# Performance work log

Hardware: AMD Instinct MI355X
Metric: run time of the kernel (lower is better)

Reference implementation:

```python
import jax, jax.numpy as jnp
import numpy as np

B, N, IN, HID, OUT = 64, 256, 7, 64, 32
DEG = 32
NT = B * N          # total nodes per side
E = NT * DEG        # intra-graph edges per side
TAU = 1.0
MAX_ITER = 10
EPS = 1e-5          # InstanceNorm2d eps


def setup_inputs() -> dict:
    key = jax.random.key(0)
    ks = jax.random.split(key, 12)

    def edges(k):
        # random intra-graph edges: local indices in [0, N) plus per-graph offset
        loc = jax.random.randint(k, (2, B, N * DEG), 0, N)
        off = (jnp.arange(B) * N)[None, :, None]
        return (loc + off).reshape(2, -1).astype(jnp.int64)

    def lin(k, fi, fo):
        return jax.random.normal(k, (fi, fo), jnp.float32) / np.float32(np.sqrt(fi))

    return {
        "x1": jax.random.normal(ks[0], (NT, IN), jnp.float32),
        "x2": jax.random.normal(ks[1], (NT, IN), jnp.float32),
        "edge1": edges(ks[2]),
        "edge2": edges(ks[3]),
        "Wl1": lin(ks[4], IN, HID), "Wr1": lin(ks[5], IN, HID),
        "bl1": jnp.zeros((HID,), jnp.float32), "br1": jnp.zeros((HID,), jnp.float32),
        "att1": jax.random.normal(ks[6], (HID,), jnp.float32) * 0.1,
        "bias1": jnp.zeros((HID,), jnp.float32),
        "Wl2": lin(ks[7], HID, OUT), "Wr2": lin(ks[8], HID, OUT),
        "bl2": jnp.zeros((OUT,), jnp.float32), "br2": jnp.zeros((OUT,), jnp.float32),
        "att2": jax.random.normal(ks[9], (OUT,), jnp.float32) * 0.1,
        "bias2": jnp.zeros((OUT,), jnp.float32),
        "gamma": jnp.ones((1,), jnp.float32),
        "beta": jnp.zeros((1,), jnp.float32),
    }


def _gatv2(x, src, dst, Wl, bl, Wr, br, att, bias):
    # PyG GATv2Conv, heads=1: score = att . leaky_relu(lin_l(x_j) + lin_r(x_i))
    xl = x @ Wl + bl  # source transform
    xr = x @ Wr + br  # target transform
    e = jax.nn.leaky_relu(xl[src] + xr[dst], 0.2)     # [E, D]
    score = e @ att                                    # [E]
    smax = jax.ops.segment_max(score, dst, num_segments=NT)
    ex = jnp.exp(score - smax[dst])
    den = jax.ops.segment_sum(ex, dst, num_segments=NT)
    alpha = ex / den[dst]
    out = jax.ops.segment_sum(alpha[:, None] * xl[src], dst, num_segments=NT)
    return out + bias


def _encode(x, edge, params):
    # add self loops (PyG add_self_loops=True default)
    loops = jnp.arange(NT)
    src = jnp.concatenate([edge[0], loops])
    dst = jnp.concatenate([edge[1], loops])
    h = jax.nn.relu(_gatv2(x, src, dst, *params[0]))
    return _gatv2(h, src, dst, *params[1])


def _soft_topk(sim_n):
    # AFAT-style differentiable top-k: OT between flattened scores and
    # {min, max} anchors with marginals [(n-k)/n, k/n], k = N2 per pair.
    n = N * N
    k = N
    flat = sim_n.reshape(B, n)
    mn = flat.min(axis=1, keepdims=True)
    mx = flat.max(axis=1, keepdims=True)
    dist = jnp.stack([flat - mn, mx - flat], axis=-1)  # [B, n, 2] (|s-min|,|s-max|)
    logK = -dist / TAU
    log_row = -jnp.log(jnp.float32(n))
    log_col = jnp.log(jnp.array([(n - k) / n, k / n], jnp.float32))
    for i in range(MAX_ITER):
        if i % 2 == 0:  # row normalization to uniform 1/n
            logK = logK - jax.scipy.special.logsumexp(logK, axis=-1, keepdims=True) + log_row
        else:           # column normalization to [(n-k)/n, k/n]
            logK = logK - jax.scipy.special.logsumexp(logK, axis=1, keepdims=True) + log_col[None, None, :]
    soft = jnp.clip(jnp.exp(logK[:, :, 1]) * n, 0.0, 1.0)  # selection probability per entry
    return soft.reshape(B, N, N)


def reference(x1, x2, edge1, edge2, Wl1, Wr1, bl1, br1, att1, bias1,
              Wl2, Wr2, bl2, br2, att2, bias2, gamma, beta):
    params = ((Wl1, bl1, Wr1, br1, att1, bias1), (Wl2, bl2, Wr2, br2, att2, bias2))
    h1 = _encode(x1, edge1, params).reshape(B, N, OUT)
    h2 = _encode(x2, edge2, params).reshape(B, N, OUT)
    sim = jnp.einsum('bnd,bmd->bnm', h1, h2)
    # InstanceNorm2d(1, affine=True): normalize each pair's sim matrix
    mu = sim.mean(axis=(1, 2), keepdims=True)
    var = sim.var(axis=(1, 2), keepdims=True)
    sim_n = gamma[0] * (sim - mu) * jax.lax.rsqrt(var + EPS) + beta[0]
    return _soft_topk(sim_n)  # soft_S stacked over the batch, [B, N, N]
```

## Files before the change

### kernel.cpp

```cpp
#include <hip/hip_runtime.h>

#define NB 64
#define NN 256
#define IND 7
#define HIDD 64
#define OUTD 32
#define EPG 8192
#define ETOT 524288
#define CAPQ 2600
#define SRCPAD 2624

typedef _Float16 f16;
typedef f16 f16x2 __attribute__((ext_vector_type(2)));
typedef f16 f16x4 __attribute__((ext_vector_type(4)));
typedef f16 f16x8 __attribute__((ext_vector_type(8)));
typedef float f32x4 __attribute__((ext_vector_type(4)));

__device__ __forceinline__ float bsum16(float v, float* rb){
#pragma unroll
  for (int o = 32; o > 0; o >>= 1) v += __shfl_xor(v, o, 64);
  __syncthreads();
  if ((threadIdx.x & 63) == 0) rb[threadIdx.x >> 6] = v;
  __syncthreads();
  float s = 0.f;
#pragma unroll
  for (int i = 0; i < 16; i++) s += rb[i];
  return s;
}
__device__ __forceinline__ float bmin16(float v, float* rb){
#pragma unroll
  for (int o = 32; o > 0; o >>= 1) v = fminf(v, __shfl_xor(v, o, 64));
  __syncthreads();
  if ((threadIdx.x & 63) == 0) rb[threadIdx.x >> 6] = v;
  __syncthreads();
  float s = rb[0];
#pragma unroll
  for (int i = 1; i < 16; i++) s = fminf(s, rb[i]);
  return s;
}
__device__ __forceinline__ float bmax16(float v, float* rb){
#pragma unroll
  for (int o = 32; o > 0; o >>= 1) v = fmaxf(v, __shfl_xor(v, o, 64));
  __syncthreads();
  if ((threadIdx.x & 63) == 0) rb[threadIdx.x >> 6] = v;
  __syncthreads();
  float s = rb[0];
#pragma unroll
  for (int i = 1; i < 16; i++) s = fmaxf(s, rb[i]);
  return s;
}

__device__ __forceinline__ f16x2 lrelu2(f16x2 s){
  const f16x2 k = {(f16)0.2f, (f16)0.2f};
  return __builtin_elementwise_max(s, s * k);
}
__device__ __forceinline__ f16x2 shfl_h2(f16x2 v, int lane){
  int i = __builtin_bit_cast(int, v);
  i = __shfl(i, lane, 64);
  return __builtin_bit_cast(f16x2, i);
}

__global__ __launch_bounds__(512, 4) void gat1(
    const float* __restrict__ x1, const float* __restrict__ x2,
    const int* __restrict__ e1, const int* __restrict__ e2,
    const float* __restrict__ Wl, const float* __restrict__ Wr,
    const float* __restrict__ bl, const float* __restrict__ br,
    const float* __restrict__ att, const float* __restrict__ bias,
    f16* __restrict__ hmid,
    int* __restrict__ meta, unsigned char* __restrict__ srcs)
{
  __shared__ __align__(16) f16 xl_s[256 * 72];
  __shared__ float sc_s[CAPQ];
  __shared__ unsigned int src_su[SRCPAD / 4];
  __shared__ int deg_s[64], start_s[64], cnt_s[64];
  unsigned char* src_s = (unsigned char*)src_su;

  const int bid = blockIdx.x;
  const int gs = bid >> 2, lo = (bid & 3) * 64;
  const int side = gs >> 6, g = gs & 63;
  const float* x = side ? x2 : x1;
  const int* eb = side ? e2 : e1;
  const int* es = eb + g * EPG;
  const int* ed = eb + ETOT + g * EPG;
  const int t = threadIdx.x;

  if (t < 64) deg_s[t] = 0;

  {
    const int node = t >> 1, dh = t & 1;
    float xv[IND];
    const float* xr_ = x + (g * 256 + node) * IND;
#pragma unroll
    for (int k = 0; k < IND; k++) xv[k] = xr_[k];
#pragma unroll
    for (int ch = 0; ch < 4; ch++){
      f16x8 o;
#pragma unroll
      for (int j = 0; j < 8; j++){
        int dd = dh * 32 + ch * 8 + j;
        float a = bl[dd];
#pragma unroll
        for (int k = 0; k < IND; k++) a = fmaf(xv[k], Wl[k * HIDD + dd], a);
        o[j] = (f16)a;
      }
      *(f16x8*)&xl_s[node * 72 + dh * 32 + ch * 8] = o;
    }
  }

  const int pairi = t >> 3, sub = t & 7, ln = lo + pairi;
  f16x2 m[4], am[4];
  {
    float xv[IND];
    const float* xq = x + (g * 256 + ln) * IND;
#pragma unroll
    for (int k = 0; k < IND; k++) xv[k] = xq[k];
#pragma unroll
    for (int c = 0; c < 4; c++){
#pragma unroll
      for (int u = 0; u < 2; u++){
        int dd = sub * 8 + 2 * c + u;
        float a = br[dd];
#pragma unroll
        for (int k = 0; k < IND; k++) a = fmaf(xv[k], Wr[k * HIDD + dd], a);
        m[c][u] = (f16)a;
        am[c][u] = (f16)att[dd];
      }
    }
  }
  f16x2 xrh[32], atth[32];
  {
    const int base = (t & 63) & ~7;
#pragma unroll
    for (int ss = 0; ss < 8; ss++){
#pragma unroll
      for (int c = 0; c < 4; c++){
        xrh[ss * 4 + c] = shfl_h2(m[c], base + ss);
        atth[ss * 4 + c] = shfl_h2(am[c], base + ss);
      }
    }
  }
  __syncthreads();

  for (int e = t; e < EPG + 256; e += 512){
    int dl = (e < EPG) ? (ed[e] & 255) : (e - EPG);
    int r = dl - lo;
    if ((unsigned)r < 64u) atomicAdd(&deg_s[r], 1);
  }
  __syncthreads();
  if (t < 64){
    int v = deg_s[t], s = v;
#pragma unroll
    for (int off = 1; off < 64; off <<= 1){
      int u = __shfl_up(s, off, 64);
      if (t >= off) s += u;
    }
    start_s[t] = s - v;
    cnt_s[t] = s - v;
    meta[bid * 128 + t] = s - v;
    meta[bid * 128 + 64 + t] = v;
  }
  __syncthreads();
  for (int e = t; e < EPG + 256; e += 512){
    int sl, dl;
    if (e < EPG){ sl = es[e] & 255; dl = ed[e] & 255; }
    else { sl = dl = e - EPG; }
    int r = dl - lo;
    if ((unsigned)r < 64u){
      int p = atomicAdd(&cnt_s[r], 1);
      if (p < CAPQ) src_s[p] = (unsigned char)sl;
    }
  }
  __syncthreads();
  {
    int ttl = start_s[63] + deg_s[63];
    if (ttl > CAPQ) ttl = CAPQ;
    unsigned int* gsrc = (unsigned int*)(srcs + (size_t)bid * SRCPAD);
    int nw = (ttl + 3) >> 2;
    for (int i = t; i < nw; i += 512) gsrc[i] = src_su[i];
  }

  const int s0 = start_s[pairi];
  int sE = s0 + deg_s[pairi];
  if (sE > CAPQ) sE = CAPQ;
  float lmax = -3.0e38f;
  for (int idx = s0 + sub; idx < sE; idx += 8){
    int sl = src_s[idx];
    const f16x8* rp = (const f16x8*)&xl_s[(unsigned)sl * 72];
    float accs[4] = {0.f, 0.f, 0.f, 0.f};
#pragma unroll
    for (int blk = 0; blk < 8; blk++){
      f16x8 rv = rp[blk];
#pragma unroll
      for (int u = 0; u < 4; u++){
        f16x2 v = {rv[2 * u], rv[2 * u + 1]};
        v = v + xrh[blk * 4 + u];
        accs[u] = __builtin_amdgcn_fdot2(lrelu2(v), atth[blk * 4 + u], accs[u], false);
      }
    }
    float sc = (accs[0] + accs[1]) + (accs[2] + accs[3]);
    sc_s[idx] = sc;
    lmax = fmaxf(lmax, sc);
  }
  lmax = fmaxf(lmax, __shfl_xor(lmax, 1, 64));
  lmax = fmaxf(lmax, __shfl_xor(lmax, 2, 64));
  lmax = fmaxf(lmax, __shfl_xor(lmax, 4, 64));
  const float smax = lmax;
  float ssum = 0.f;
  for (int idx = s0 + sub; idx < sE; idx += 8){
    float w = __expf(sc_s[idx] - smax);
    ssum += w;
    sc_s[idx] = w;
  }
  ssum += __shfl_xor(ssum, 1, 64);
  ssum += __shfl_xor(ssum, 2, 64);
  ssum += __shfl_xor(ssum, 4, 64);
  float inv = 1.f / ssum;
  float acc[8];
#pragma unroll
  for (int c = 0; c < 8; c++) acc[c] = 0.f;
  {
    int sl = (s0 < sE) ? src_s[s0] : 0;
    f16x8 row = *(const f16x8*)&xl_s[(unsigned)sl * 72 + sub * 8];
    for (int idx = s0; idx < sE; idx++){
      int sln = (idx + 1 < sE) ? src_s[idx + 1] : 0;
      f16x8 rown = *(const f16x8*)&xl_s[(unsigned)sln * 72 + sub * 8];
      float w = sc_s[idx];
#pragma unroll
      for (int c = 0; c < 8; c++) acc[c] = fmaf(w, (float)row[c], acc[c]);
      row = rown;
    }
  }
  f16x8 o;
#pragma unroll
  for (int c = 0; c < 8; c++)
    o[c] = (f16)fmaxf(acc[c] * inv + bias[sub * 8 + c], 0.f);
  *(f16x8*)(hmid + (size_t)(gs * 256 + ln) * 64 + sub * 8) = o;
}

__global__ __launch_bounds__(512, 4) void gat2(
    const int* __restrict__ meta, const unsigned char* __restrict__ srcs,
    const f16* __restrict__ hmid,
    const float* __restrict__ Wl, const float* __restrict__ Wr,
    const float* __restrict__ bl, const float* __restrict__ br,
    const float* __restrict__ att, const float* __restrict__ bias,
    f16* __restrict__ hout)
{
  __shared__ __align__(16) f16 xl_s[256 * 40];
  __shared__ __align__(16) f16 xr_s[64 * 40];
  __shared__ float sc_s[CAPQ];
  __shared__ unsigned int src_su[SRCPAD / 4];
  __shared__ int start_s[64], deg_s[64];
  unsigned char* src_s = (unsigned char*)src_su;

  const int bid = blockIdx.x;
  const int gs = bid >> 2, lo = (bid & 3) * 64;
  const int t = threadIdx.x;

  if (t < 64){
    start_s[t] = meta[bid * 128 + t];
    deg_s[t] = meta[bid * 128 + 64 + t];
  }
  {
    int ttl = meta[bid * 128 + 63] + meta[bid * 128 + 64 + 63];
    if (ttl > CAPQ) ttl = CAPQ;
    const unsigned int* gsrc = (const unsigned int*)(srcs + (size_t)bid * SRCPAD);
    int nw = (ttl + 3) >> 2;
    for (int i = t; i < nw; i += 512) src_su[i] = gsrc[i];
  }

  {
    const int w = t >> 6, lane = t & 63;
    const int m = lane & 15, quad = lane >> 4;
    f16x8 a[2][2];
#pragma unroll
    for (int ti = 0; ti < 2; ti++){
      const f16* arow = hmid + (size_t)(gs * 256 + (2 * w + ti) * 16 + m) * 64;
      a[ti][0] = *(const f16x8*)(arow + quad * 8);
      a[ti][1] = *(const f16x8*)(arow + 32 + quad * 8);
    }
#pragma unroll
    for (int H = 0; H < 2; H++){
      const int n = H * 16 + m;
      f16x8 b0, b1;
#pragma unroll
      for (int j = 0; j < 8; j++){
        b0[j] = (f16)Wl[(quad * 8 + j) * 32 + n];
        b1[j] = (f16)Wl[(32 + quad * 8 + j) * 32 + n];
      }
      const float bv = bl[n];
#pragma unroll
      for (int ti = 0; ti < 2; ti++){
        f32x4 acc = {0.f, 0.f, 0.f, 0.f};
        acc = __builtin_amdgcn_mfma_f32_16x16x32_f16(a[ti][0], b0, acc, 0, 0, 0);
        acc = __builtin_amdgcn_mfma_f32_16x16x32_f16(a[ti][1], b1, acc, 0, 0, 0);
#pragma unroll
        for (int r = 0; r < 4; r++)
          xl_s[((2 * w + ti) * 16 + quad * 4 + r) * 40 + n] = (f16)(acc[r] + bv);
      }
    }
    if (w < 4){
      const f16* arow = hmid + (size_t)(gs * 256 + lo + w * 16 + m) * 64;
      f16x8 c0 = *(const f16x8*)(arow + quad * 8);
      f16x8 c1 = *(const f16x8*)(arow + 32 + quad * 8);
#pragma unroll
      for (int H = 0; H < 2; H++){
        const int n = H * 16 + m;
        f16x8 b0, b1;
#pragma unroll
        for (int j = 0; j < 8; j++){
          b0[j] = (f16)Wr[(quad * 8 + j) * 32 + n];
          b1[j] = (f16)Wr[(32 + quad * 8 + j) * 32 + n];
        }
        const float bv = br[n];
        f32x4 acc = {0.f, 0.f, 0.f, 0.f};
        acc = __builtin_amdgcn_mfma_f32_16x16x32_f16(c0, b0, acc, 0, 0, 0);
        acc = __builtin_amdgcn_mfma_f32_16x16x32_f16(c1, b1, acc, 0, 0, 0);
#pragma unroll
        for (int r = 0; r < 4; r++)
          xr_s[(w * 16 + quad * 4 + r) * 40 + n] = (f16)(acc[r] + bv);
      }
    }
  }
  __syncthreads();

  const int pairi = t >> 3, sub = t & 7, ln = lo + pairi;
  f16x2 xrh[16], atth[16];
  {
    const f16x8* xrp = (const f16x8*)&xr_s[pairi * 40];
#pragma unroll
    for (int q = 0; q < 4; q++){
      f16x8 v = xrp[q];
#pragma unroll
      for (int u = 0; u < 4; u++){
        xrh[q * 4 + u][0] = v[2 * u];
        xrh[q * 4 + u][1] = v[2 * u + 1];
      }
    }
#pragma unroll
    for (int i = 0; i < 16; i++){
      atth[i][0] = (f16)att[2 * i];
      atth[i][1] = (f16)att[2 * i + 1];
    }
  }

  const int s0 = start_s[pairi];
  int sE = s0 + deg_s[pairi];
  if (sE > CAPQ) sE = CAPQ;
  float lmax = -3.0e38f;
  for (int idx = s0 + sub; idx < sE; idx += 8){
    int sl = src_s[idx];
    const f16x8* rp = (const f16x8*)&xl_s[(unsigned)sl * 40];
    float accs[4] = {0.f, 0.f, 0.f, 0.f};
#pragma unroll
    for (int blk = 0; blk < 4; blk++){
      f16x8 rv = rp[blk];
#pragma unroll
      for (int u = 0; u < 4; u++){
        f16x2 v = {rv[2 * u], rv[2 * u + 1]};
        v = v + xrh[blk * 4 + u];
        accs[u] = __builtin_amdgcn_fdot2(lrelu2(v), atth[blk * 4 + u], accs[u], false);
      }
    }
    float sc = (accs[0] + accs[1]) + (accs[2] + accs[3]);
    sc_s[idx] = sc;
    lmax = fmaxf(lmax, sc);
  }
  lmax = fmaxf(lmax, __shfl_xor(lmax, 1, 64));
  lmax = fmaxf(lmax, __shfl_xor(lmax, 2, 64));
  lmax = fmaxf(lmax, __shfl_xor(lmax, 4, 64));
  const float smax = lmax;
  float ssum = 0.f;
  for (int idx = s0 + sub; idx < sE; idx += 8){
    float w = __expf(sc_s[idx] - smax);
    ssum += w;
    sc_s[idx] = w;
  }
  ssum += __shfl_xor(ssum, 1, 64);
  ssum += __shfl_xor(ssum, 2, 64);
  ssum += __shfl_xor(ssum, 4, 64);
  float inv = 1.f / ssum;

  float acc[4];
#pragma unroll
  for (int c = 0; c < 4; c++) acc[c] = 0.f;
  {
    int sl = (s0 < sE) ? src_s[s0] : 0;
    f16x4 row = *(const f16x4*)&xl_s[(unsigned)sl * 40 + sub * 4];
    for (int idx = s0; idx < sE; idx++){
      int sln = (idx + 1 < sE) ? src_s[idx + 1] : 0;
      f16x4 rown = *(const f16x4*)&xl_s[(unsigned)sln * 40 + sub * 4];
      float w = sc_s[idx];
#pragma unroll
      for (int c = 0; c < 4; c++) acc[c] = fmaf(w, (float)row[c], acc[c]);
      row = rown;
    }
  }
  f16x4 o;
#pragma unroll
  for (int c = 0; c < 4; c++)
    o[c] = (f16)(acc[c] * inv + bias[sub * 4 + c]);
  *(f16x4*)(hout + (size_t)(gs * 256 + ln) * 32 + sub * 4) = o;
}

__global__ __launch_bounds__(1024) void simtopk(
    const f16* __restrict__ H,
    const float* __restrict__ gamma, const float* __restrict__ beta,
    float* __restrict__ out)
{
  __shared__ float rb[16];
  __shared__ unsigned int hist[8192];
  const int b = blockIdx.x, t = threadIdx.x;
  const int w = t >> 6, lane = t & 63;
  const int m = lane & 15, quad = lane >> 4;

  const f16* h1 = H + (size_t)b * 256 * 32;
  const f16* h2 = H + (size_t)(64 + b) * 256 * 32;

  f16x8 av = *(const f16x8*)(h1 + (size_t)(w * 16 + m) * 32 + quad * 8);
  f32x4 c[16];
#pragma unroll
  for (int j = 0; j < 16; j++){
    f16x8 bv = *(const f16x8*)(h2 + (size_t)(j * 16 + m) * 32 + quad * 8);
    f32x4 z = {0.f, 0.f, 0.f, 0.f};
    c[j] = __builtin_amdgcn_mfma_f32_16x16x32_f16(av, bv, z, 0, 0, 0);
  }

  float sm = 0.f, s2 = 0.f, mn = 3.0e38f, mx = -3.0e38f;
#pragma unroll
  for (int j = 0; j < 16; j++)
#pragma unroll
    for (int r = 0; r < 4; r++){
      float s = c[j][r];
      sm += s; s2 = fmaf(s, s, s2);
      mn = fminf(mn, s); mx = fmaxf(mx, s);
    }
  sm = bsum16(sm, rb);
  s2 = bsum16(s2, rb);
  mn = bmin16(mn, rb);
  mx = bmax16(mx, rb);

  const float mu = sm * (1.f / 65536.f);
  const float var = s2 * (1.f / 65536.f) - mu * mu;
  const float a = gamma[0] * rsqrtf(var + 1e-5f);
  const float cc = beta[0] - a * mu;
  float mnn = a * mn + cc, mxn = a * mx + cc;
  if (a < 0.f){ float tmp = mnn; mnn = mxn; mxn = tmp; }
  const float al = 2.f * a;
  const float be = 2.f * cc - mnn - mxn;
  const float R = fmaxf(mxn - mnn, 1e-12f);
  const float binscale = 4096.f / R;

  for (int i = t; i < 8192; i += 1024) hist[i] = 0u;
  __syncthreads();
#pragma unroll
  for (int j = 0; j < 16; j++)
#pragma unroll
    for (int r = 0; r < 4; r++){
      float z = fmaf(al, c[j][r], be);
      int bi = (int)fmaf(z, binscale, 4096.f);
      bi = min(max(bi, 0), 8191);
      atomicAdd(&hist[bi], 1u);
      c[j][r] = __expf(-z);
    }
  __syncthreads();

  const float wbin = R * (1.f / 4096.f);
  float ebs[8];
#pragma unroll
  for (int j = 0; j < 8; j++){
    float zc = fmaf((float)(t * 8 + j) + 0.5f, wbin, -R);
    ebs[j] = __expf(-zc);
  }
  float cnts[8];
#pragma unroll
  for (int j = 0; j < 8; j++) cnts[j] = (float)hist[t * 8 + j];

  float D = 0.f, S = 256.f, eD = 1.f;
  for (int p = 0; p < 5; p++){
    float loc = 0.f;
#pragma unroll
    for (int j = 0; j < 8; j++)
      loc += cnts[j] / (1.f + ebs[j] * eD);
    S = bsum16(loc, rb);
    if (p < 4){
      D += -5.5412635f  + __logf(65536.f - S) - __logf(S);
      eD = __expf(-D);
    }
  }

  const float scale = 256.f / S;
  float* ob = out + (size_t)b * 65536;
#pragma unroll
  for (int j = 0; j < 16; j++){
#pragma unroll
    for (int r = 0; r < 4; r++){
      float v = scale / (1.f + c[j][r] * eD);
      int row = w * 16 + quad * 4 + r;
      int col = j * 16 + m;
      ob[row * 256 + col] = fminf(v, 1.f);
    }
  }
}

extern "C" void kernel_launch(void* const* d_in, const int* in_sizes, int n_in,
                              void* d_out, int out_size, void* d_ws, size_t ws_size,
                              hipStream_t stream)
{
  const float* x1   = (const float*)d_in[0];
  const float* x2   = (const float*)d_in[1];
  const int*   e1   = (const int*)d_in[2];
  const int*   e2   = (const int*)d_in[3];
  const float* Wl1  = (const float*)d_in[4];
  const float* Wr1  = (const float*)d_in[5];
  const float* bl1  = (const float*)d_in[6];
  const float* br1  = (const float*)d_in[7];
  const float* att1 = (const float*)d_in[8];
  const float* bias1= (const float*)d_in[9];
  const float* Wl2  = (const float*)d_in[10];
  const float* Wr2  = (const float*)d_in[11];
  const float* bl2  = (const float*)d_in[12];
  const float* br2  = (const float*)d_in[13];
  const float* att2 = (const float*)d_in[14];
  const float* bias2= (const float*)d_in[15];
  const float* gamma= (const float*)d_in[16];
  const float* beta = (const float*)d_in[17];

  char* ws = (char*)d_ws;
  f16* hmid = (f16*)ws;
  f16* hfin = (f16*)(ws + (size_t)4 * 1024 * 1024);
  int* meta = (int*)(ws + (size_t)6 * 1024 * 1024);
  unsigned char* srcs = (unsigned char*)(ws + (size_t)6 * 1024 * 1024 + 512 * 128 * 4);
  float* out = (float*)d_out;

  gat1<<<512, 512, 0, stream>>>(x1, x2, e1, e2, Wl1, Wr1, bl1, br1, att1, bias1,
                                hmid, meta, srcs);
  gat2<<<512, 512, 0, stream>>>(meta, srcs, hmid, Wl2, Wr2, bl2, br2, att2, bias2, hfin);
  simtopk<<<64, 1024, 0, stream>>>(hfin, gamma, beta, out);
}
```

Measured before the change: 188.1 us.

## Split sim/topk into multi-kernel pipeline and degree-sort destination nodes in GAT

The single 64-block sim+Sinkhorn kernel becomes three stages: a 256-block matmul kernel that writes raw similarities and atomically combines per-batch statistics, a histogram/Sinkhorn-solve kernel that reads sim back, and a 512-block elementwise output kernel. The aim is to use more CUs than 64 blocks could. In exchange the 16 MB output is written, read and rewritten through global memory, with extra launches and a zeroing kernel. The GAT kernels also cache edge indices in registers so edges are read from global memory once. They sort destination nodes by degree so that the 8-lane groups sharing a wavefront have similar work, reducing divergence.

```diff
diff --git a/kernel.cpp b/kernel.cpp
--- a/kernel.cpp
+++ b/kernel.cpp
@@ -58,6 +58,14 @@
   int i = __builtin_bit_cast(int, v);
   i = __shfl(i, lane, 64);
   return __builtin_bit_cast(f16x2, i);
+}
+__device__ __forceinline__ unsigned fkey(float f){
+  unsigned b = __float_as_uint(f);
+  return (b & 0x80000000u) ? ~b : (b | 0x80000000u);
+}
+__device__ __forceinline__ float fkinv(unsigned k){
+  unsigned b = (k & 0x80000000u) ? (k ^ 0x80000000u) : ~k;
+  return __uint_as_float(b);
 }
 
 __global__ __launch_bounds__(512, 4) void gat1(
@@ -73,6 +81,7 @@
   __shared__ float sc_s[CAPQ];
   __shared__ unsigned int src_su[SRCPAD / 4];
   __shared__ int deg_s[64], start_s[64], cnt_s[64];
+  __shared__ unsigned char perm[64];
   unsigned char* src_s = (unsigned char*)src_su;
 
   const int bid = blockIdx.x;
@@ -86,6 +95,20 @@
 
   if (t < 64) deg_s[t] = 0;
 
+  unsigned short epk[17];
+  int nE = 0;
+#pragma unroll
+  for (int i = 0; i < 17; i++){
+    int e = t + i * 512;
+    if (e < EPG + 256){
+      int sl, dl;
+      if (e < EPG){ sl = es[e] & 255; dl = ed[e] & 255; }
+      else { sl = dl = e - EPG; }
+      epk[i] = (unsigned short)((dl << 8) | sl);
+      nE = i + 1;
+    }
+  }
+
   {
     const int node = t >> 1, dh = t & 1;
     float xv[IND];
@@ -106,44 +129,11 @@
       *(f16x8*)&xl_s[node * 72 + dh * 32 + ch * 8] = o;
     }
   }
-
-  const int pairi = t >> 3, sub = t & 7, ln = lo + pairi;
-  f16x2 m[4], am[4];
-  {
-    float xv[IND];
-    const float* xq = x + (g * 256 + ln) * IND;
-#pragma unroll
-    for (int k = 0; k < IND; k++) xv[k] = xq[k];
-#pragma unroll
-    for (int c = 0; c < 4; c++){
-#pragma unroll
-      for (int u = 0; u < 2; u++){
-        int dd = sub * 8 + 2 * c + u;
-        float a = br[dd];
-#pragma unroll
-        for (int k = 0; k < IND; k++) a = fmaf(xv[k], Wr[k * HIDD + dd], a);
-        m[c][u] = (f16)a;
-        am[c][u] = (f16)att[dd];
-      }
-    }
-  }
-  f16x2 xrh[32], atth[32];
-  {
-    const int base = (t & 63) & ~7;
-#pragma unroll
-    for (int ss = 0; ss < 8; ss++){
-#pragma unroll
-      for (int c = 0; c < 4; c++){
-        xrh[ss * 4 + c] = shfl_h2(m[c], base + ss);
-        atth[ss * 4 + c] = shfl_h2(am[c], base + ss);
-      }
-    }
-  }
-  __syncthreads();
-
-  for (int e = t; e < EPG + 256; e += 512){
-    int dl = (e < EPG) ? (ed[e] & 255) : (e - EPG);
-    int r = dl - lo;
+  __syncthreads();
+
+#pragma unroll
+  for (int i = 0; i < 17; i++) if (i < nE){
+    int r = (epk[i] >> 8) - lo;
     if ((unsigned)r < 64u) atomicAdd(&deg_s[r], 1);
   }
   __syncthreads();
@@ -158,16 +148,21 @@
     cnt_s[t] = s - v;
     meta[bid * 128 + t] = s - v;
     meta[bid * 128 + 64 + t] = v;
-  }
-  __syncthreads();
-  for (int e = t; e < EPG + 256; e += 512){
-    int sl, dl;
-    if (e < EPG){ sl = es[e] & 255; dl = ed[e] & 255; }
-    else { sl = dl = e - EPG; }
-    int r = dl - lo;
+    int r = 0;
+#pragma unroll 8
+    for (int j = 0; j < 64; j++){
+      int dj = deg_s[j];
+      r += (dj < v) || (dj == v && j < t);
+    }
+    perm[r] = (unsigned char)t;
+  }
+  __syncthreads();
+#pragma unroll
+  for (int i = 0; i < 17; i++) if (i < nE){
+    int dl = epk[i] >> 8, r = dl - lo;
     if ((unsigned)r < 64u){
       int p = atomicAdd(&cnt_s[r], 1);
-      if (p < CAPQ) src_s[p] = (unsigned char)sl;
+      if (p < CAPQ) src_s[p] = (unsigned char)(epk[i] & 255);
     }
   }
   __syncthreads();
@@ -177,6 +172,39 @@
     unsigned int* gsrc = (unsigned int*)(srcs + (size_t)bid * SRCPAD);
     int nw = (ttl + 3) >> 2;
     for (int i = t; i < nw; i += 512) gsrc[i] = src_su[i];
+  }
+
+  const int pairi = perm[t >> 3], sub = t & 7, ln = lo + pairi;
+  f16x2 m[4], am[4];
+  {
+    float xv[IND];
+    const float* xq = x + (g * 256 + ln) * IND;
+#pragma unroll
+    for (int k = 0; k < IND; k++) xv[k] = xq[k];
+#pragma unroll
+    for (int c = 0; c < 4; c++){
+#pragma unroll
+      for (int u = 0; u < 2; u++){
+        int dd = sub * 8 + 2 * c + u;
+        float a = br[dd];
+#pragma unroll
+        for (int k = 0; k < IND; k++) a = fmaf(xv[k], Wr[k * HIDD + dd], a);
+        m[c][u] = (f16)a;
+        am[c][u] = (f16)att[dd];
+      }
+    }
+  }
+  f16x2 xrh[32], atth[32];
+  {
+    const int base = (t & 63) & ~7;
+#pragma unroll
+    for (int ss = 0; ss < 8; ss++){
+#pragma unroll
+      for (int c = 0; c < 4; c++){
+        xrh[ss * 4 + c] = shfl_h2(m[c], base + ss);
+        atth[ss * 4 + c] = shfl_h2(am[c], base + ss);
+      }
+    }
   }
 
   const int s0 = start_s[pairi];
@@ -250,6 +278,7 @@
   __shared__ float sc_s[CAPQ];
   __shared__ unsigned int src_su[SRCPAD / 4];
   __shared__ int start_s[64], deg_s[64];
+  __shared__ unsigned char perm[64];
   unsigned char* src_s = (unsigned char*)src_su;
 
   const int bid = blockIdx.x;
@@ -322,8 +351,18 @@
     }
   }
   __syncthreads();
-
-  const int pairi = t >> 3, sub = t & 7, ln = lo + pairi;
+  if (t < 64){
+    int v = deg_s[t], r = 0;
+#pragma unroll 8
+    for (int j = 0; j < 64; j++){
+      int dj = deg_s[j];
+      r += (dj < v) || (dj == v && j < t);
+    }
+    perm[r] = (unsigned char)t;
+  }
+  __syncthreads();
+
+  const int pairi = perm[t >> 3], sub = t & 7, ln = lo + pairi;
   f16x2 xrh[16], atth[16];
   {
     const f16x8* xrp = (const f16x8*)&xr_s[pairi * 40];
@@ -402,45 +441,73 @@
   *(f16x4*)(hout + (size_t)(gs * 256 + ln) * 32 + sub * 4) = o;
 }
 
-__global__ __launch_bounds__(1024) void simtopk(
-    const f16* __restrict__ H,
+__global__ __launch_bounds__(256) void zerok(unsigned* __restrict__ stats){
+  int i = threadIdx.x;
+  if (i < 256) stats[i] = ((i & 3) == 2) ? 0xFFFFFFFFu : 0u;
+}
+
+__global__ __launch_bounds__(1024) void simk(
+    const f16* __restrict__ H, float* __restrict__ out,
+    unsigned* __restrict__ stats)
+{
+  __shared__ float rb[16];
+  const int b = blockIdx.x >> 2, q = blockIdx.x & 3, t = threadIdx.x;
+  const int w = t >> 6, lane = t & 63;
+  const int m = lane & 15, quad = lane >> 4;
+  const int rowT = q * 64 + (w & 3) * 16;
+  const int colB = (w >> 2) * 64;
+
+  const f16* h1 = H + (size_t)b * 256 * 32;
+  const f16* h2 = H + (size_t)(64 + b) * 256 * 32;
+
+  f16x8 av = *(const f16x8*)(h1 + (size_t)(rowT + m) * 32 + quad * 8);
+  f32x4 c[4];
+#pragma unroll
+  for (int jj = 0; jj < 4; jj++){
+    f16x8 bv = *(const f16x8*)(h2 + (size_t)(colB + jj * 16 + m) * 32 + quad * 8);
+    f32x4 z = {0.f, 0.f, 0.f, 0.f};
+    c[jj] = __builtin_amdgcn_mfma_f32_16x16x32_f16(av, bv, z, 0, 0, 0);
+  }
+
+  float sm = 0.f, s2 = 0.f, mn = 3.0e38f, mx = -3.0e38f;
+  float* ob = out + (size_t)b * 65536;
+#pragma unroll
+  for (int jj = 0; jj < 4; jj++)
+#pragma unroll
+    for (int r = 0; r < 4; r++){
+      float s = c[jj][r];
+      sm += s; s2 = fmaf(s, s, s2);
+      mn = fminf(mn, s); mx = fmaxf(mx, s);
+      ob[(rowT + quad * 4 + r) * 256 + colB + jj * 16 + m] = s;
+    }
+  sm = bsum16(sm, rb);
+  s2 = bsum16(s2, rb);
+  mn = bmin16(mn, rb);
+  mx = bmax16(mx, rb);
+  if (t == 0){
+    atomicAdd((float*)&stats[b * 4 + 0], sm);
+    atomicAdd((float*)&stats[b * 4 + 1], s2);
+    atomicMin(&stats[b * 4 + 2], fkey(mn));
+    atomicMax(&stats[b * 4 + 3], fkey(mx));
+  }
+}
+
+__global__ __launch_bounds__(1024) void sinkk(
+    const float* __restrict__ sim, const unsigned* __restrict__ stats,
     const float* __restrict__ gamma, const float* __restrict__ beta,
-    float* __restrict__ out)
+    float* __restrict__ res)
 {
   __shared__ float rb[16];
   __shared__ unsigned int hist[8192];
   const int b = blockIdx.x, t = threadIdx.x;
-  const int w = t >> 6, lane = t & 63;
-  const int m = lane & 15, quad = lane >> 4;
-
-  const f16* h1 = H + (size_t)b * 256 * 32;
-  const f16* h2 = H + (size_t)(64 + b) * 256 * 32;
-
-  f16x8 av = *(const f16x8*)(h1 + (size_t)(w * 16 + m) * 32 + quad * 8);
-  f32x4 c[16];
-#pragma unroll
-  for (int j = 0; j < 16; j++){
-    f16x8 bv = *(const f16x8*)(h2 + (size_t)(j * 16 + m) * 32 + quad * 8);
-    f32x4 z = {0.f, 0.f, 0.f, 0.f};
-    c[j] = __builtin_amdgcn_mfma_f32_16x16x32_f16(av, bv, z, 0, 0, 0);
-  }
-
-  float sm = 0.f, s2 = 0.f, mn = 3.0e38f, mx = -3.0e38f;
-#pragma unroll
-  for (int j = 0; j < 16; j++)
-#pragma unroll
-    for (int r = 0; r < 4; r++){
-      float s = c[j][r];
-      sm += s; s2 = fmaf(s, s, s2);
-      mn = fminf(mn, s); mx = fmaxf(mx, s);
-    }
-  sm = bsum16(sm, rb);
-  s2 = bsum16(s2, rb);
-  mn = bmin16(mn, rb);
-  mx = bmax16(mx, rb);
-
-  const float mu = sm * (1.f / 65536.f);
-  const float var = s2 * (1.f / 65536.f) - mu * mu;
+
+  const float sum = __uint_as_float(stats[b * 4 + 0]);
+  const float ssq = __uint_as_float(stats[b * 4 + 1]);
+  const float mn = fkinv(stats[b * 4 + 2]);
+  const float mx = fkinv(stats[b * 4 + 3]);
+
+  const float mu = sum * (1.f / 65536.f);
+  const float var = ssq * (1.f / 65536.f) - mu * mu;
   const float a = gamma[0] * rsqrtf(var + 1e-5f);
   const float cc = beta[0] - a * mu;
   float mnn = a * mn + cc, mxn = a * mx + cc;
@@ -452,28 +519,28 @@
 
   for (int i = t; i < 8192; i += 1024) hist[i] = 0u;
   __syncthreads();
-#pragma unroll
-  for (int j = 0; j < 16; j++)
-#pragma unroll
-    for (int r = 0; r < 4; r++){
-      float z = fmaf(al, c[j][r], be);
+  const f32x4* sp = (const f32x4*)(sim + (size_t)b * 65536);
+#pragma unroll
+  for (int k = 0; k < 16; k++){
+    f32x4 v = sp[k * 1024 + t];
+#pragma unroll
+    for (int u = 0; u < 4; u++){
+      float z = fmaf(al, v[u], be);
       int bi = (int)fmaf(z, binscale, 4096.f);
       bi = min(max(bi, 0), 8191);
       atomicAdd(&hist[bi], 1u);
-      c[j][r] = __expf(-z);
-    }
+    }
+  }
   __syncthreads();
 
   const float wbin = R * (1.f / 4096.f);
-  float ebs[8];
+  float ebs[8], cnts[8];
 #pragma unroll
   for (int j = 0; j < 8; j++){
     float zc = fmaf((float)(t * 8 + j) + 0.5f, wbin, -R);
     ebs[j] = __expf(-zc);
-  }
-  float cnts[8];
-#pragma unroll
-  for (int j = 0; j < 8; j++) cnts[j] = (float)hist[t * 8 + j];
+    cnts[j] = (float)hist[t * 8 + j];
+  }
 
   float D = 0.f, S = 256.f, eD = 1.f;
   for (int p = 0; p < 5; p++){
@@ -487,18 +554,30 @@
       eD = __expf(-D);
     }
   }
-
-  const float scale = 256.f / S;
-  float* ob = out + (size_t)b * 65536;
-#pragma unroll
-  for (int j = 0; j < 16; j++){
-#pragma unroll
-    for (int r = 0; r < 4; r++){
-      float v = scale / (1.f + c[j][r] * eD);
-      int row = w * 16 + quad * 4 + r;
-      int col = j * 16 + m;
-      ob[row * 256 + col] = fminf(v, 1.f);
-    }
+  if (t == 0){
+    res[b * 4 + 0] = al;
+    res[b * 4 + 1] = be + D;
+    res[b * 4 + 2] = 256.f / S;
+  }
+}
+
+__global__ __launch_bounds__(256) void outk(
+    float* __restrict__ out, const float* __restrict__ res)
+{
+  const int b = blockIdx.x >> 3, seg = blockIdx.x & 7, t = threadIdx.x;
+  const float al = res[b * 4 + 0];
+  const float beD = res[b * 4 + 1];
+  const float scale = res[b * 4 + 2];
+  f32x4* p = (f32x4*)(out + (size_t)b * 65536 + seg * 8192);
+#pragma unroll
+  for (int k = 0; k < 8; k++){
+    f32x4 v = p[k * 256 + t];
+#pragma unroll
+    for (int u = 0; u < 4; u++){
+      float z = fmaf(al, v[u], beD);
+      v[u] = fminf(scale / (1.f + __expf(-z)), 1.f);
+    }
+    p[k * 256 + t] = v;
   }
 }
 
@@ -530,10 +609,15 @@
   f16* hfin = (f16*)(ws + (size_t)4 * 1024 * 1024);
   int* meta = (int*)(ws + (size_t)6 * 1024 * 1024);
   unsigned char* srcs = (unsigned char*)(ws + (size_t)6 * 1024 * 1024 + 512 * 128 * 4);
+  unsigned* stats = (unsigned*)(ws + (size_t)8 * 1024 * 1024);
+  float* res = (float*)(ws + (size_t)8 * 1024 * 1024 + 4096);
   float* out = (float*)d_out;
 
+  zerok<<<1, 256, 0, stream>>>(stats);
   gat1<<<512, 512, 0, stream>>>(x1, x2, e1, e2, Wl1, Wr1, bl1, br1, att1, bias1,
                                 hmid, meta, srcs);
   gat2<<<512, 512, 0, stream>>>(meta, srcs, hmid, Wl2, Wr2, bl2, br2, att2, bias2, hfin);
-  simtopk<<<64, 1024, 0, stream>>>(hfin, gamma, beta, out);
-}
+  simk<<<256, 1024, 0, stream>>>(hfin, out, stats);
+  sinkk<<<64, 1024, 0, stream>>>(out, stats, gamma, beta, res);
+  outk<<<512, 256, 0, stream>>>(out, res);
+}
```

New measurement: 190.8 us. No clear change (+1.4%).
